# Performance work log

Hardware: AMD Instinct MI355X
Metric: run time of the kernel (lower is better)

The kernel has to match this reference:

```python
import jax, jax.numpy as jnp
import numpy as np

OUT_H, OUT_W = 7, 7
SPATIAL_SCALE = 0.125
SAMPLING_RATIO = 2


def setup_inputs() -> dict:
    key = jax.random.key(0)
    k1, k2, k3, k4 = jax.random.split(key, 4)
    inputs = jax.random.normal(k1, (2, 100, 100, 256), dtype=jnp.float32)
    # boxes in image coords (stride-8 feature over ~800px image): x0,y0,x1,y1
    xy0 = jax.random.uniform(k2, (1024, 2), minval=0.0, maxval=600.0)
    wh = jax.random.uniform(k3, (1024, 2), minval=8.0, maxval=200.0)
    boxes = jnp.concatenate([xy0, xy0 + wh], axis=1).astype(jnp.float32)
    box_inds = jax.random.randint(k4, (1024,), 0, 2, dtype=jnp.int32)
    return {"inputs": inputs, "boxes": boxes, "box_inds": box_inds}


def _roi_align(inputs, boxes, box_inds):
    """aligned=True ROIAlign: crop_and_resize at oversampled grid + avg pool.

    Sample coordinate (per aligned=True transform + tf.crop_and_resize):
      x_j = x0*scale + spacing_w*(j+0.5) - 0.5, spacing_w = w_box*scale/crop_w
    Out-of-range samples get extrapolation_value=0 (TF semantics).
    """
    N, H, W, C = inputs.shape
    B = boxes.shape[0]
    ch, cw = OUT_H * SAMPLING_RATIO, OUT_W * SAMPLING_RATIO

    sb = boxes * SPATIAL_SCALE
    x0, y0, x1, y1 = sb[:, 0], sb[:, 1], sb[:, 2], sb[:, 3]
    sw = (x1 - x0) / cw  # [B]
    sh = (y1 - y0) / ch
    xs = x0[:, None] + sw[:, None] * (jnp.arange(cw, dtype=sb.dtype) + 0.5) - 0.5  # [B,cw]
    ys = y0[:, None] + sh[:, None] * (jnp.arange(ch, dtype=sb.dtype) + 0.5) - 0.5  # [B,ch]

    yl = jnp.floor(ys)
    xl = jnp.floor(xs)
    ty = ys - yl  # [B,ch]
    tx = xs - xl  # [B,cw]
    yli = jnp.clip(yl, 0, H - 1).astype(jnp.int32)
    yhi = jnp.clip(yl + 1, 0, H - 1).astype(jnp.int32)
    xli = jnp.clip(xl, 0, W - 1).astype(jnp.int32)
    xhi = jnp.clip(xl + 1, 0, W - 1).astype(jnp.int32)

    b = box_inds[:, None, None]

    def g(yy, xx):  # gather -> [B,ch,cw,C]
        return inputs[b, yy[:, :, None], xx[:, None, :], :]

    txe = tx[:, None, :, None]
    top = g(yli, xli) * (1.0 - txe) + g(yli, xhi) * txe
    bot = g(yhi, xli) * (1.0 - txe) + g(yhi, xhi) * txe
    tye = ty[:, :, None, None]
    out = top * (1.0 - tye) + bot * tye  # [B,ch,cw,C]

    valid = ((ys >= 0) & (ys <= H - 1))[:, :, None] & ((xs >= 0) & (xs <= W - 1))[:, None, :]
    out = jnp.where(valid[..., None], out, 0.0)

    # avg_pool2d kernel=stride=SAMPLING_RATIO (SAME==VALID since exact multiple)
    out = out.reshape(B, OUT_H, SAMPLING_RATIO, OUT_W, SAMPLING_RATIO, C).mean(axis=(2, 4))
    return out  # [B, OUT_H, OUT_W, C]


def reference(inputs, boxes, box_inds):
    return _roi_align(inputs, boxes, box_inds)
```

## Files before the change

kernel.cpp:

```cpp
#include <hip/hip_runtime.h>


constexpr int   H_IN  = 100;
constexpr int   W_IN  = 100;
constexpr int   C_IN  = 256;
constexpr int   OUT_H = 7;
constexpr int   OUT_W = 7;
constexpr int   NPIX  = OUT_H * OUT_W;
constexpr int   NBOX  = 1024;
constexpr float SCALE = 0.125f;

typedef float f32x4 __attribute__((ext_vector_type(4)));

constexpr int PMETA_OFF = 4096;

__global__ __launch_bounds__(1024) void sort_boxes_kernel(
    const float* __restrict__ boxes,
    const int*   __restrict__ box_inds,
    int*         __restrict__ perm)
{
    const int tid  = threadIdx.x;
    const int wave = tid >> 6;
    const int lane = tid & 63;

    const float y0 = boxes[tid * 4 + 1] * SCALE;
    const float y1 = boxes[tid * 4 + 3] * SCALE;
    const float cy = 0.5f * (y0 + y1);
    int band = (int)(cy * (1.0f / 25.0f));
    band = min(max(band, 0), 3);
    const int bin = box_inds[tid] * 4 + band;

    __shared__ int whist[16][8];
    __shared__ int sc[129];

    int wrank = 0;
    const unsigned long long ltmask = (lane == 63) ? ~0ull >> 1
                                                   : (1ull << lane) - 1;
#pragma unroll
    for (int k = 0; k < 8; ++k) {
        const unsigned long long bal = __ballot(bin == k);
        if (bin == k) wrank = __popcll(bal & ltmask);
        if (lane == 0) whist[wave][k] = __popcll(bal);
    }
    __syncthreads();

    if (tid < 128) sc[tid + 1] = whist[tid & 15][tid >> 4];
    if (tid == 0)  sc[0] = 0;
    __syncthreads();
    for (int off = 1; off < 128; off <<= 1) {
        int v = 0;
        if (tid < 128 && tid >= off) v = sc[tid - off + 1];
        __syncthreads();
        if (tid < 128 && tid >= off) sc[tid + 1] += v;
        __syncthreads();
    }

    perm[sc[bin * 16 + wave] + wrank] = tid;
}

__device__ __forceinline__ void fold_dim(float s0, float step, int LIM,
                                         int& c0, int& n, float* w)
{
    float s[2] = { s0, s0 + step };
    int   fl[2]; float t[2]; bool val[2];
    int lo = 0x7fffffff, hi = -0x7fffffff;
#pragma unroll
    for (int k = 0; k < 2; ++k) {
        const float f = floorf(s[k]);
        fl[k]  = (int)f;
        t[k]   = s[k] - f;
        val[k] = (s[k] >= 0.0f && s[k] <= (float)(LIM - 1));
        if (val[k]) {
            lo = min(lo, fl[k]);
            hi = max(hi, min(fl[k] + 1, LIM - 1));
        }
    }
    w[0] = w[1] = w[2] = w[3] = 0.0f;
    if (lo > hi) {
        c0 = min(max(fl[0], 0), LIM - 1);
        n  = 1;
        return;
    }
    c0 = lo;
    n  = hi - lo + 1;
#pragma unroll
    for (int k = 0; k < 2; ++k) {
        if (val[k]) {
            w[fl[k] - lo]                    += 1.0f - t[k];
            w[min(fl[k] + 1, LIM - 1) - lo]  += t[k];
        }
    }
}

__global__ __launch_bounds__(256) void pmeta_kernel(
    const float* __restrict__ boxes,
    const int*   __restrict__ box_inds,
    const int*   __restrict__ perm,
    int*         __restrict__ pm)
{
    const int p = blockIdx.x * 256 + threadIdx.x;
    if (p >= NBOX * NPIX) return;
    const int slot = p / NPIX;
    const int rem  = p - slot * NPIX;
    const int oy   = (rem * 37) >> 8;
    const int ox   = rem - oy * 7;

    const int b = perm[slot];
    const int n = box_inds[b];

    const float bx0 = boxes[b * 4 + 0] * SCALE;
    const float by0 = boxes[b * 4 + 1] * SCALE;
    const float bx1 = boxes[b * 4 + 2] * SCALE;
    const float by1 = boxes[b * 4 + 3] * SCALE;
    const float sw  = (bx1 - bx0) * (1.0f / 14.0f);
    const float sh  = (by1 - by0) * (1.0f / 14.0f);

    int r0, nr; float wr[4];
    fold_dim(by0 + sh * ((float)(oy * 2) + 0.5f) - 0.5f, sh, H_IN, r0, nr, wr);
    int c0, nc; float wc[4];
    fold_dim(bx0 + sw * ((float)(ox * 2) + 0.5f) - 0.5f, sw, W_IN, c0, nc, wc);

    int* q = pm + p * 12;
    q[0] = n * (H_IN * W_IN * C_IN) + r0 * (W_IN * C_IN) + c0 * C_IN;
    q[1] = (b * NPIX + rem) * C_IN;
    q[2] = (nr - 1) * 4 + (nc - 1);
    q[3] = 0;
    float* qf = (float*)q;
    qf[4] = wr[0] * 0.25f; qf[5] = wr[1] * 0.25f;
    qf[6] = wr[2] * 0.25f; qf[7] = wr[3] * 0.25f;
    qf[8] = wc[0]; qf[9] = wc[1]; qf[10] = wc[2]; qf[11] = wc[3];
}

template<int NR, int NC>
__device__ __forceinline__ f32x4 gather(const float* __restrict__ src,
                                        const float* wr, const float* wc)
{
    f32x4 v[NR][NC];
#pragma unroll
    for (int i = 0; i < NR; ++i)
#pragma unroll
        for (int j = 0; j < NC; ++j)
            v[i][j] = *(const f32x4*)(src + i * (W_IN * C_IN) + j * C_IN);

    f32x4 acc = {0.f, 0.f, 0.f, 0.f};
#pragma unroll
    for (int i = 0; i < NR; ++i)
#pragma unroll
        for (int j = 0; j < NC; ++j)
            acc += v[i][j] * (wr[i] * wc[j]);
    return acc;
}

__global__ __launch_bounds__(256) void roi_align_kernel(
    const float* __restrict__ inputs,
    const int*   __restrict__ pm,
    float*       __restrict__ out)
{
    __shared__ int smeta[48];

    const int tid  = threadIdx.x;
    const int lane = tid & 63;
    const int wv   = tid >> 6;

    const int nchunk = gridDim.x >> 3;
    const int lbid   = (blockIdx.x & 7) * nchunk + (blockIdx.x >> 3);
    const int p0     = lbid * 4;

    if (tid < 48) smeta[tid] = pm[p0 * 12 + tid];
    __syncthreads();

    const int* m = smeta + wv * 12;
    const int  base = m[0];
    const int  oute = m[1];
    const int  sel  = __builtin_amdgcn_readfirstlane(m[2]);
    const float* wr = (const float*)(m + 4);
    const float* wc = (const float*)(m + 8);

    const float* src = inputs + base + lane * 4;

    f32x4 acc;
    switch (sel) {
        case 0:  acc = gather<1, 1>(src, wr, wc); break;
        case 1:  acc = gather<1, 2>(src, wr, wc); break;
        case 2:  acc = gather<1, 3>(src, wr, wc); break;
        case 3:  acc = gather<1, 4>(src, wr, wc); break;
        case 4:  acc = gather<2, 1>(src, wr, wc); break;
        case 5:  acc = gather<2, 2>(src, wr, wc); break;
        case 6:  acc = gather<2, 3>(src, wr, wc); break;
        case 7:  acc = gather<2, 4>(src, wr, wc); break;
        case 8:  acc = gather<3, 1>(src, wr, wc); break;
        case 9:  acc = gather<3, 2>(src, wr, wc); break;
        case 10: acc = gather<3, 3>(src, wr, wc); break;
        case 11: acc = gather<3, 4>(src, wr, wc); break;
        case 12: acc = gather<4, 1>(src, wr, wc); break;
        case 13: acc = gather<4, 2>(src, wr, wc); break;
        case 14: acc = gather<4, 3>(src, wr, wc); break;
        default: acc = gather<4, 4>(src, wr, wc); break;
    }

    __builtin_nontemporal_store(acc, (f32x4*)(out + oute + lane * 4));
}

extern "C" void kernel_launch(void* const* d_in, const int* in_sizes, int n_in,
                              void* d_out, int out_size, void* d_ws, size_t ws_size,
                              hipStream_t stream) {
    const float* inputs   = (const float*)d_in[0];
    const float* boxes    = (const float*)d_in[1];
    const int*   box_inds = (const int*)d_in[2];
    float*       out      = (float*)d_out;

    int* perm = (int*)d_ws;
    int* pm   = (int*)((char*)d_ws + PMETA_OFF);

    sort_boxes_kernel<<<1, NBOX, 0, stream>>>(boxes, box_inds, perm);
    pmeta_kernel<<<196, 256, 0, stream>>>(boxes, box_inds, perm, pm);

    const int blocks = NBOX * NPIX / 4;
    roi_align_kernel<<<blocks, 256, 0, stream>>>(inputs, pm, out);
}
```

Before: 33.14 us.

## Merge sort and metadata kernels into one prep kernel with separable row/col metadata

Folds the box sort and per-pixel metadata computation into a single one-block prep kernel, which removes a kernel launch and the global perm round trip. The per-pixel 48-byte metadata is replaced by separable per-row and per-column records (7+7 per box instead of 49), and the main kernel combines them itself. This removes the shared-memory staging and barrier in the main kernel. In exchange, all metadata work now runs on one 1024-thread block, serializing 14 iterations on a single CU, and the main kernel does two dependent metadata loads per wave.

```diff
diff --git a/kernel.cpp b/kernel.cpp
--- a/kernel.cpp
+++ b/kernel.cpp
@@ -12,51 +12,9 @@
 
 typedef float f32x4 __attribute__((ext_vector_type(4)));
 
-constexpr int PMETA_OFF = 4096;
-
-__global__ __launch_bounds__(1024) void sort_boxes_kernel(
-    const float* __restrict__ boxes,
-    const int*   __restrict__ box_inds,
-    int*         __restrict__ perm)
-{
-    const int tid  = threadIdx.x;
-    const int wave = tid >> 6;
-    const int lane = tid & 63;
-
-    const float y0 = boxes[tid * 4 + 1] * SCALE;
-    const float y1 = boxes[tid * 4 + 3] * SCALE;
-    const float cy = 0.5f * (y0 + y1);
-    int band = (int)(cy * (1.0f / 25.0f));
-    band = min(max(band, 0), 3);
-    const int bin = box_inds[tid] * 4 + band;
-
-    __shared__ int whist[16][8];
-    __shared__ int sc[129];
-
-    int wrank = 0;
-    const unsigned long long ltmask = (lane == 63) ? ~0ull >> 1
-                                                   : (1ull << lane) - 1;
-#pragma unroll
-    for (int k = 0; k < 8; ++k) {
-        const unsigned long long bal = __ballot(bin == k);
-        if (bin == k) wrank = __popcll(bal & ltmask);
-        if (lane == 0) whist[wave][k] = __popcll(bal);
-    }
-    __syncthreads();
-
-    if (tid < 128) sc[tid + 1] = whist[tid & 15][tid >> 4];
-    if (tid == 0)  sc[0] = 0;
-    __syncthreads();
-    for (int off = 1; off < 128; off <<= 1) {
-        int v = 0;
-        if (tid < 128 && tid >= off) v = sc[tid - off + 1];
-        __syncthreads();
-        if (tid < 128 && tid >= off) sc[tid + 1] += v;
-        __syncthreads();
-    }
-
-    perm[sc[bin * 16 + wave] + wrank] = tid;
-}
+struct Meta { int4 off; float4 w; };
+
+constexpr int CMETA_OFF = 7168 * 32;
 
 __device__ __forceinline__ void fold_dim(float s0, float step, int LIM,
                                          int& c0, int& n, float* w)
@@ -92,91 +50,143 @@
     }
 }
 
-__global__ __launch_bounds__(256) void pmeta_kernel(
+__global__ __launch_bounds__(1024) void prep_kernel(
     const float* __restrict__ boxes,
     const int*   __restrict__ box_inds,
-    const int*   __restrict__ perm,
-    int*         __restrict__ pm)
-{
-    const int p = blockIdx.x * 256 + threadIdx.x;
-    if (p >= NBOX * NPIX) return;
+    Meta*        __restrict__ rmeta,
+    Meta*        __restrict__ cmeta)
+{
+    const int tid  = threadIdx.x;
+    const int wave = tid >> 6;
+    const int lane = tid & 63;
+
+    __shared__ int whist[16][8];
+    __shared__ int sc[128];
+    __shared__ int sperm[NBOX];
+
+    const float by0 = boxes[tid * 4 + 1] * SCALE;
+    const float by1 = boxes[tid * 4 + 3] * SCALE;
+    const float cy  = 0.5f * (by0 + by1);
+    int band = (int)(cy * (1.0f / 25.0f));
+    band = min(max(band, 0), 3);
+    const int bin = box_inds[tid] * 4 + band;
+
+    int wrank = 0;
+    const unsigned long long ltmask = (lane == 63) ? ~0ull >> 1
+                                                   : (1ull << lane) - 1;
+#pragma unroll
+    for (int k = 0; k < 8; ++k) {
+        const unsigned long long bal = __ballot(bin == k);
+        if (bin == k) wrank = __popcll(bal & ltmask);
+        if (lane == 0) whist[wave][k] = __popcll(bal);
+    }
+    __syncthreads();
+
+    if (wave == 0) {
+        const int e0 = 2 * lane, e1 = 2 * lane + 1;
+        const int a = whist[e0 & 15][e0 >> 4];
+        const int bq = whist[e1 & 15][e1 >> 4];
+        int v = a + bq;
+        int incl = v;
+#pragma unroll
+        for (int d = 1; d < 64; d <<= 1) {
+            const int t = __shfl_up(incl, d, 64);
+            if (lane >= d) incl += t;
+        }
+        const int base = incl - v;
+        sc[e0] = base;
+        sc[e1] = base + a;
+    }
+    __syncthreads();
+
+    sperm[sc[bin * 16 + wave] + wrank] = tid;
+    __syncthreads();
+
+#pragma unroll 1
+    for (int k = 0; k < 14; ++k) {
+        const int item = k * 1024 + tid;
+        const int slot = item / 14;
+        const int d    = item - slot * 14;
+
+        const int b = sperm[slot];
+        const int n = box_inds[b];
+        const float4 bx = ((const float4*)boxes)[b];
+        const float x0 = bx.x * SCALE, y0 = bx.y * SCALE;
+        const float x1 = bx.z * SCALE, y1 = bx.w * SCALE;
+        const float sw = (x1 - x0) * (1.0f / 14.0f);
+        const float sh = (y1 - y0) * (1.0f / 14.0f);
+
+        int c0, cnt; float wgt[4];
+        Meta m;
+        m.off.z = 0; m.off.w = 0;
+        if (d < 7) {
+            fold_dim(y0 + sh * ((float)(d * 2) + 0.5f) - 0.5f, sh, H_IN,
+                     c0, cnt, wgt);
+            m.off.x = (n * (H_IN * W_IN * C_IN) + c0 * (W_IN * C_IN)) | (cnt - 1);
+            m.off.y = (b * NPIX + d * OUT_W) * C_IN;
+            m.w.x = wgt[0] * 0.25f; m.w.y = wgt[1] * 0.25f;
+            m.w.z = wgt[2] * 0.25f; m.w.w = wgt[3] * 0.25f;
+            rmeta[slot * 7 + d] = m;
+        } else {
+            fold_dim(x0 + sw * ((float)((d - 7) * 2) + 0.5f) - 0.5f, sw, W_IN,
+                     c0, cnt, wgt);
+            m.off.x = (c0 * C_IN) | (cnt - 1);
+            m.off.y = 0;
+            m.w.x = wgt[0]; m.w.y = wgt[1]; m.w.z = wgt[2]; m.w.w = wgt[3];
+            cmeta[slot * 7 + (d - 7)] = m;
+        }
+    }
+}
+
+template<int NR, int NC>
+__device__ __forceinline__ f32x4 gather(const float* __restrict__ src,
+                                        const float* wr, const float* wc)
+{
+    f32x4 v[NR][NC];
+#pragma unroll
+    for (int i = 0; i < NR; ++i)
+#pragma unroll
+        for (int j = 0; j < NC; ++j)
+            v[i][j] = *(const f32x4*)(src + i * (W_IN * C_IN) + j * C_IN);
+
+    f32x4 acc = {0.f, 0.f, 0.f, 0.f};
+#pragma unroll
+    for (int i = 0; i < NR; ++i)
+#pragma unroll
+        for (int j = 0; j < NC; ++j)
+            acc += v[i][j] * (wr[i] * wc[j]);
+    return acc;
+}
+
+__global__ __launch_bounds__(256) void roi_align_kernel(
+    const float* __restrict__ inputs,
+    const Meta*  __restrict__ rmeta,
+    const Meta*  __restrict__ cmeta,
+    float*       __restrict__ out)
+{
+    const int lane = threadIdx.x & 63;
+    const int sub  = __builtin_amdgcn_readfirstlane(threadIdx.x >> 6);
+
+    const int nchunk = gridDim.x >> 3;
+    const int lbid   = (blockIdx.x & 7) * nchunk + (blockIdx.x >> 3);
+    const int p      = lbid * 4 + sub;
+
     const int slot = p / NPIX;
     const int rem  = p - slot * NPIX;
     const int oy   = (rem * 37) >> 8;
     const int ox   = rem - oy * 7;
 
-    const int b = perm[slot];
-    const int n = box_inds[b];
-
-    const float bx0 = boxes[b * 4 + 0] * SCALE;
-    const float by0 = boxes[b * 4 + 1] * SCALE;
-    const float bx1 = boxes[b * 4 + 2] * SCALE;
-    const float by1 = boxes[b * 4 + 3] * SCALE;
-    const float sw  = (bx1 - bx0) * (1.0f / 14.0f);
-    const float sh  = (by1 - by0) * (1.0f / 14.0f);
-
-    int r0, nr; float wr[4];
-    fold_dim(by0 + sh * ((float)(oy * 2) + 0.5f) - 0.5f, sh, H_IN, r0, nr, wr);
-    int c0, nc; float wc[4];
-    fold_dim(bx0 + sw * ((float)(ox * 2) + 0.5f) - 0.5f, sw, W_IN, c0, nc, wc);
-
-    int* q = pm + p * 12;
-    q[0] = n * (H_IN * W_IN * C_IN) + r0 * (W_IN * C_IN) + c0 * C_IN;
-    q[1] = (b * NPIX + rem) * C_IN;
-    q[2] = (nr - 1) * 4 + (nc - 1);
-    q[3] = 0;
-    float* qf = (float*)q;
-    qf[4] = wr[0] * 0.25f; qf[5] = wr[1] * 0.25f;
-    qf[6] = wr[2] * 0.25f; qf[7] = wr[3] * 0.25f;
-    qf[8] = wc[0]; qf[9] = wc[1]; qf[10] = wc[2]; qf[11] = wc[3];
-}
-
-template<int NR, int NC>
-__device__ __forceinline__ f32x4 gather(const float* __restrict__ src,
-                                        const float* wr, const float* wc)
-{
-    f32x4 v[NR][NC];
-#pragma unroll
-    for (int i = 0; i < NR; ++i)
-#pragma unroll
-        for (int j = 0; j < NC; ++j)
-            v[i][j] = *(const f32x4*)(src + i * (W_IN * C_IN) + j * C_IN);
-
-    f32x4 acc = {0.f, 0.f, 0.f, 0.f};
-#pragma unroll
-    for (int i = 0; i < NR; ++i)
-#pragma unroll
-        for (int j = 0; j < NC; ++j)
-            acc += v[i][j] * (wr[i] * wc[j]);
-    return acc;
-}
-
-__global__ __launch_bounds__(256) void roi_align_kernel(
-    const float* __restrict__ inputs,
-    const int*   __restrict__ pm,
-    float*       __restrict__ out)
-{
-    __shared__ int smeta[48];
-
-    const int tid  = threadIdx.x;
-    const int lane = tid & 63;
-    const int wv   = tid >> 6;
-
-    const int nchunk = gridDim.x >> 3;
-    const int lbid   = (blockIdx.x & 7) * nchunk + (blockIdx.x >> 3);
-    const int p0     = lbid * 4;
-
-    if (tid < 48) smeta[tid] = pm[p0 * 12 + tid];
-    __syncthreads();
-
-    const int* m = smeta + wv * 12;
-    const int  base = m[0];
-    const int  oute = m[1];
-    const int  sel  = __builtin_amdgcn_readfirstlane(m[2]);
-    const float* wr = (const float*)(m + 4);
-    const float* wc = (const float*)(m + 8);
-
-    const float* src = inputs + base + lane * 4;
+    const Meta rm = rmeta[slot * 7 + oy];
+    const Meta cm = cmeta[slot * 7 + ox];
+
+    const int rpk = __builtin_amdgcn_readfirstlane(rm.off.x);
+    const int cpk = __builtin_amdgcn_readfirstlane(cm.off.x);
+    const int sel = (rpk & 3) * 4 + (cpk & 3);
+
+    const float wr[4] = { rm.w.x, rm.w.y, rm.w.z, rm.w.w };
+    const float wc[4] = { cm.w.x, cm.w.y, cm.w.z, cm.w.w };
+
+    const float* src = inputs + (rpk & ~3) + (cpk & ~3) + lane * 4;
 
     f32x4 acc;
     switch (sel) {
@@ -198,7 +208,8 @@
         default: acc = gather<4, 4>(src, wr, wc); break;
     }
 
-    __builtin_nontemporal_store(acc, (f32x4*)(out + oute + lane * 4));
+    float* op = out + rm.off.y + ox * C_IN + lane * 4;
+    __builtin_nontemporal_store(acc, (f32x4*)op);
 }
 
 extern "C" void kernel_launch(void* const* d_in, const int* in_sizes, int n_in,
@@ -209,12 +220,11 @@
     const int*   box_inds = (const int*)d_in[2];
     float*       out      = (float*)d_out;
 
-    int* perm = (int*)d_ws;
-    int* pm   = (int*)((char*)d_ws + PMETA_OFF);
-
-    sort_boxes_kernel<<<1, NBOX, 0, stream>>>(boxes, box_inds, perm);
-    pmeta_kernel<<<196, 256, 0, stream>>>(boxes, box_inds, perm, pm);
+    Meta* rmeta = (Meta*)d_ws;
+    Meta* cmeta = (Meta*)((char*)d_ws + CMETA_OFF);
+
+    prep_kernel<<<1, NBOX, 0, stream>>>(boxes, box_inds, rmeta, cmeta);
 
     const int blocks = NBOX * NPIX / 4;
-    roi_align_kernel<<<blocks, 256, 0, stream>>>(inputs, pm, out);
-}
+    roi_align_kernel<<<blocks, 256, 0, stream>>>(inputs, rmeta, cmeta, out);
+}
```

Measured after the change: 47.82 us. +44.3%, slower.
